# Kernel tuning notes

Measured on AMD Instinct MI355X. Metric: run time of the kernel, lower is better.

The kernel has to match this reference:

```python
import jax, jax.numpy as jnp
import numpy as np

B, H, W, C, A, K = 1_000_000, 4, 4, 3, 4, 20
# slicing offsets (w_offset, h_offset) exactly as in the torch code
OFFSETS = [(0, 1), (2, 1), (1, 0), (1, 2)]


def setup_inputs() -> dict:
    key = jax.random.key(0)
    k0, k1, k2, k3, k4, k5 = jax.random.split(key, 6)
    obs = jax.random.normal(k0, (B, H, W, C), dtype=jnp.float32)
    # channel 1 encodes the agent position: exactly one nonzero per sample
    pos = jax.random.randint(k1, (B,), 0, H * W)
    ch1 = jnp.zeros((B, H * W), jnp.float32).at[jnp.arange(B), pos].set(1.0)
    obs = obs.at[..., 1].set(ch1.reshape(B, H, W)).reshape(B, H * W * C)
    s = 0.05  # keep |p| < 1 mostly so the K-step VI recursion stays bounded
    return {
        'obs': obs,
        'Phi_W': jax.random.normal(k2, (48, 48), jnp.float32) * s,
        'Phi_b': jax.random.normal(k3, (48,), jnp.float32) * s,
        'Logit_W': jax.random.normal(k4, (A, 36), jnp.float32) * s,
        'Logit_b': jax.random.normal(k5, (A,), jnp.float32) * s,
    }


def _pad2(x):
    # zero-pad last two spatial dims of (B, H, W) by 1
    return jnp.pad(x, ((0, 0), (1, 1), (1, 1)))


def reference(obs, Phi_W, Phi_b, Logit_W, Logit_b):
    out = (obs @ Phi_W.T + Phi_b).reshape(B, H, W, C)
    rin, rout, p = out[..., 0], out[..., 1], out[..., 2]
    rin_pad = _pad2(rin)  # (B, 6, 6)

    def step(v, _):
        vp = _pad2(v)  # (B, 6, 6)
        for wo, ho in OFFSETS:
            nv = p * vp[:, ho:ho + H, wo:wo + W] + rin_pad[:, ho:ho + H, wo:wo + W] - rout
            v = jnp.maximum(v, nv)
        return v, None

    V, _ = jax.lax.scan(step, jnp.zeros((B, H, W), jnp.float32), None, length=K)

    # agent position: first nonzero of channel 1 (row-major), default (1,1) -> flat 5
    obs4 = obs.reshape(B, H, W, C)
    nz = (obs4[..., 1] != 0).reshape(B, H * W)
    idx = jnp.where(nz.any(axis=1), jnp.argmax(nz, axis=1), 5)
    i, j = idx // W, idx % W

    # 3x3 windows around (i, j) in zero-padded state / value maps
    obs_pad = jnp.pad(obs4, ((0, 0), (1, 1), (1, 1), (0, 0)))  # (B, 6, 6, 3)
    V_pad = _pad2(V)                                            # (B, 6, 6)
    d = jnp.arange(3)
    rows = i[:, None, None] + d[:, None]   # (B, 3, 1)
    cols = j[:, None, None] + d[None, :]   # (B, 1, 3)
    bb = jnp.arange(B)[:, None, None]
    sub_state = obs_pad[bb, rows, cols]    # (B, 3, 3, 3)
    sub_v = V_pad[bb, rows, cols]          # (B, 3, 3)

    logit_in = jnp.concatenate([sub_state.reshape(B, 27), sub_v.reshape(B, 9)], axis=1)
    logit = logit_in @ Logit_W.T + Logit_b  # (B, A)
    return logit
```

## Files before the change

### kernel.cpp

```cpp
#include <hip/hip_runtime.h>
#include <hip/hip_bf16.h>

#define BT 256
#define WREG 13312

typedef __attribute__((ext_vector_type(8))) short short8;
typedef __attribute__((ext_vector_type(4))) float f32x4;

__device__ inline short f2b(float x) {
    return __builtin_bit_cast(short, __float2bfloat16(x));
}
__device__ inline float b2f(short s) {
    unsigned u = ((unsigned)(unsigned short)s) << 16;
    return __builtin_bit_cast(float, u);
}
__device__ inline short8 pack8(float4 a, float4 b) {
    short8 r;
    r[0] = f2b(a.x); r[1] = f2b(a.y); r[2] = f2b(a.z); r[3] = f2b(a.w);
    r[4] = f2b(b.x); r[5] = f2b(b.y); r[6] = f2b(b.z); r[7] = f2b(b.w);
    return r;
}

__global__ __launch_bounds__(BT, 3) void vin_kernel(
    const float* __restrict__ obs,
    const float* __restrict__ PhiW,
    const float* __restrict__ Phib,
    const float* __restrict__ LW,
    const float* __restrict__ Lb,
    float* __restrict__ out, int Btot)
{
    __shared__ __align__(16) char smem[4 * WREG];
    const int tid  = threadIdx.x;
    const int lane = tid & 63;
    const int wid  = tid >> 6;
    const int b    = blockIdx.x * BT + tid;
    if (b >= Btot) return;

    char* wbase = smem + wid * WREG;
    const int jn = lane & 15;
    const int g  = lane >> 4;

    float o[48];
    {
        const float4* g4 = reinterpret_cast<const float4*>(obs + (size_t)b * 48);
        #pragma unroll
        for (int q = 0; q < 12; ++q) {
            float4 t = g4[q];
            o[4*q+0] = t.x; o[4*q+1] = t.y; o[4*q+2] = t.z; o[4*q+3] = t.w;
        }
    }

    int idx = 5;
    #pragma unroll
    for (int k = 15; k >= 0; --k)
        if (o[k*3+1] != 0.0f) idx = k;
    const int ai = idx >> 2;
    const int aj = idx & 3;

    short8 bfrag[3][2];
    #pragma unroll
    for (int n = 0; n < 3; ++n) {
        const float* wrow = PhiW + (16*n + jn) * 48;
        float4 q0 = *reinterpret_cast<const float4*>(wrow + 8*g);
        float4 q1 = *reinterpret_cast<const float4*>(wrow + 8*g + 4);
        bfrag[n][0] = pack8(q0, q1);
        short8 z = {0,0,0,0,0,0,0,0};
        if (g < 2) {
            float4 q2 = *reinterpret_cast<const float4*>(wrow + 32 + 8*g);
            float4 q3 = *reinterpret_cast<const float4*>(wrow + 36 + 8*g);
            z = pack8(q2, q3);
        }
        bfrag[n][1] = z;
    }

    {
        short8* arow = reinterpret_cast<short8*>(wbase + lane * 144);
        #pragma unroll
        for (int t = 0; t < 6; ++t) {
            short8 v;
            #pragma unroll
            for (int e = 0; e < 8; ++e) v[e] = f2b(o[t*8 + e]);
            arow[t] = v;
        }
        short8 z = {0,0,0,0,0,0,0,0};
        arow[6] = z; arow[7] = z;
    }

    float lg0 = Lb[0], lg1 = Lb[1], lg2 = Lb[2], lg3 = Lb[3];
    {
        const short* myobs = reinterpret_cast<const short*>(wbase + lane * 144);
        #pragma unroll
        for (int dh = 0; dh < 3; ++dh) {
            #pragma unroll
            for (int dw = 0; dw < 3; ++dw) {
                int r = ai + dh - 1, c = aj + dw - 1;
                bool ok = ((unsigned)r < 4u) && ((unsigned)c < 4u);
                int ba = ok ? (r*4 + c) * 3 : 0;
                float s0 = b2f(myobs[ba+0]);
                float s1 = b2f(myobs[ba+1]);
                float s2 = b2f(myobs[ba+2]);
                if (!ok) { s0 = 0.f; s1 = 0.f; s2 = 0.f; }
                int f = (dh*3 + dw) * 3;
                lg0 = fmaf(s0, LW[0*36+f], fmaf(s1, LW[0*36+f+1], fmaf(s2, LW[0*36+f+2], lg0)));
                lg1 = fmaf(s0, LW[1*36+f], fmaf(s1, LW[1*36+f+1], fmaf(s2, LW[1*36+f+2], lg1)));
                lg2 = fmaf(s0, LW[2*36+f], fmaf(s1, LW[2*36+f+1], fmaf(s2, LW[2*36+f+2], lg2)));
                lg3 = fmaf(s0, LW[3*36+f], fmaf(s1, LW[3*36+f+1], fmaf(s2, LW[3*36+f+2], lg3)));
            }
        }
    }

    short8 afrag[4][2];
    #pragma unroll
    for (int m = 0; m < 4; ++m) {
        const char* rp = wbase + (m*16 + jn) * 144;
        afrag[m][0] = *reinterpret_cast<const short8*>(rp + 16*g);
        afrag[m][1] = *reinterpret_cast<const short8*>(rp + 64 + 16*g);
    }

    f32x4 acc[4][3];
    #pragma unroll
    for (int m = 0; m < 4; ++m)
        #pragma unroll
        for (int n = 0; n < 3; ++n)
            acc[m][n] = (f32x4){0.f, 0.f, 0.f, 0.f};
    #pragma unroll
    for (int n = 0; n < 3; ++n)
        #pragma unroll
        for (int m = 0; m < 4; ++m) {
            acc[m][n] = __builtin_amdgcn_mfma_f32_16x16x32_bf16(afrag[m][0], bfrag[n][0], acc[m][n], 0, 0, 0);
            acc[m][n] = __builtin_amdgcn_mfma_f32_16x16x32_bf16(afrag[m][1], bfrag[n][1], acc[m][n], 0, 0, 0);
        }

    asm volatile("s_waitcnt lgkmcnt(0)" ::: "memory");
    __builtin_amdgcn_sched_barrier(0);

    #pragma unroll
    for (int m = 0; m < 4; ++m)
        #pragma unroll
        for (int n = 0; n < 3; ++n)
            #pragma unroll
            for (int r = 0; r < 4; ++r) {
                int row = m*16 + g*4 + r;
                reinterpret_cast<float*>(wbase + row * 208)[n*16 + jn] = acc[m][n][r];
            }

    asm volatile("s_waitcnt lgkmcnt(0)" ::: "memory");
    __builtin_amdgcn_sched_barrier(0);

    float ro[48];
    {
        const char* myrow = wbase + lane * 208;
        #pragma unroll
        for (int q = 0; q < 12; ++q) {
            f32x4 t = *reinterpret_cast<const f32x4*>(myrow + q * 16);
            ro[4*q+0] = t[0] + Phib[4*q+0];
            ro[4*q+1] = t[1] + Phib[4*q+1];
            ro[4*q+2] = t[2] + Phib[4*q+2];
            ro[4*q+3] = t[3] + Phib[4*q+3];
        }
    }

    float pc[16], aL[16], aR[16], aU[16], aD[16];
    #pragma unroll
    for (int h = 0; h < 4; ++h)
        #pragma unroll
        for (int w = 0; w < 4; ++w) {
            int cl = h*4 + w;
            float rout = ro[cl*3 + 1];
            pc[cl] = ro[cl*3 + 2];
            aL[cl] = ((w > 0) ? ro[(cl-1)*3] : 0.0f) - rout;
            aR[cl] = ((w < 3) ? ro[(cl+1)*3] : 0.0f) - rout;
            aU[cl] = ((h > 0) ? ro[(cl-4)*3] : 0.0f) - rout;
            aD[cl] = ((h < 3) ? ro[(cl+4)*3] : 0.0f) - rout;
        }

    float V[16];
    #pragma unroll
    for (int k = 0; k < 16; ++k) V[k] = 0.0f;

    #pragma unroll 1
    for (int s = 0; s < 20; ++s) {
        float Vn[16];
        #pragma unroll
        for (int h = 0; h < 4; ++h)
            #pragma unroll
            for (int w = 0; w < 4; ++w) {
                int cl = h*4 + w;
                float cL = (w > 0) ? fmaf(pc[cl], V[cl-1], aL[cl]) : aL[cl];
                float cR = (w < 3) ? fmaf(pc[cl], V[cl+1], aR[cl]) : aR[cl];
                float cU = (h > 0) ? fmaf(pc[cl], V[cl-4], aU[cl]) : aU[cl];
                float cD = (h < 3) ? fmaf(pc[cl], V[cl+4], aD[cl]) : aD[cl];
                Vn[cl] = fmaxf(fmaxf(V[cl], cL), fmaxf(fmaxf(cR, cU), cD));
            }
        #pragma unroll
        for (int k = 0; k < 16; ++k) V[k] = Vn[k];
    }

    {
        char* myrow = wbase + lane * 208;
        #pragma unroll
        for (int q = 0; q < 4; ++q)
            *reinterpret_cast<f32x4*>(myrow + q * 16) =
                (f32x4){V[4*q+0], V[4*q+1], V[4*q+2], V[4*q+3]};
    }
    asm volatile("s_waitcnt lgkmcnt(0)" ::: "memory");
    __builtin_amdgcn_sched_barrier(0);
    {
        const float* myv = reinterpret_cast<const float*>(wbase + lane * 208);
        #pragma unroll
        for (int dh = 0; dh < 3; ++dh)
            #pragma unroll
            for (int dw = 0; dw < 3; ++dw) {
                int r = ai + dh - 1, c = aj + dw - 1;
                bool ok = ((unsigned)r < 4u) && ((unsigned)c < 4u);
                int ba = ok ? (r*4 + c) : 0;
                float v = myv[ba];
                if (!ok) v = 0.0f;
                int f = 27 + dh*3 + dw;
                lg0 = fmaf(v, LW[0*36+f], lg0);
                lg1 = fmaf(v, LW[1*36+f], lg1);
                lg2 = fmaf(v, LW[2*36+f], lg2);
                lg3 = fmaf(v, LW[3*36+f], lg3);
            }
    }

    reinterpret_cast<float4*>(out)[b] = make_float4(lg0, lg1, lg2, lg3);
}

extern "C" void kernel_launch(void* const* d_in, const int* in_sizes, int n_in,
                              void* d_out, int out_size, void* d_ws, size_t ws_size,
                              hipStream_t stream) {
    const float* obs  = (const float*)d_in[0];
    const float* PhiW = (const float*)d_in[1];
    const float* Phib = (const float*)d_in[2];
    const float* LW   = (const float*)d_in[3];
    const float* Lb   = (const float*)d_in[4];
    float* out = (float*)d_out;

    const int Btot = in_sizes[0] / 48;
    const int grid = (Btot + BT - 1) / BT;
    hipLaunchKernelGGL(vin_kernel, dim3(grid), dim3(BT), 0, stream,
                       obs, PhiW, Phib, LW, Lb, out, Btot);
}
```

Measured before the change: 73.97 us.

## Run value iteration in packed fp16, pre-convert PhiW to bf16, fold bias into MFMA

Runs the 20-step value iteration in packed half2 arithmetic, two grid cells per register, with bit shifts supplying horizontal neighbours. This roughly halves the VALU work in the main loop. A small prep kernel converts PhiW to a padded bf16 layout in workspace, so each thread loads its B fragments directly instead of converting them. Other changes: the bias is folded into the MFMA accumulator initialisation, bf16 packing uses manual rounding, and the agent-index search becomes an arithmetic weighted sum. The fp16 recursion lowers accuracy. The weighted-sum index only works because channel 1 holds exactly one 1.0, so it relies on the input format.

```diff
diff --git a/kernel.cpp b/kernel.cpp
--- a/kernel.cpp
+++ b/kernel.cpp
@@ -1,29 +1,41 @@
 #include <hip/hip_runtime.h>
-#include <hip/hip_bf16.h>
 
 #define BT 256
 #define WREG 13312
 
 typedef __attribute__((ext_vector_type(8))) short short8;
 typedef __attribute__((ext_vector_type(4))) float f32x4;
-
-__device__ inline short f2b(float x) {
-    return __builtin_bit_cast(short, __float2bfloat16(x));
+typedef __attribute__((ext_vector_type(4))) unsigned int u32x4;
+typedef _Float16 h2 __attribute__((ext_vector_type(2)));
+
+__device__ inline h2 hfma2(h2 a, h2 b, h2 c) { return __builtin_elementwise_fma(a, b, c); }
+__device__ inline h2 hmax2(h2 a, h2 b)       { return __builtin_elementwise_max(a, b); }
+__device__ inline h2 mkh2(float a, float b)  { h2 r; r[0] = (_Float16)a; r[1] = (_Float16)b; return r; }
+
+__device__ inline unsigned bf16r(float x) {
+    unsigned u = __builtin_bit_cast(unsigned, x);
+    return (u + 0x7FFFu + ((u >> 16) & 1u)) >> 16;
+}
+__device__ inline unsigned pk2bf(float a, float b) {
+    return bf16r(a) | (bf16r(b) << 16);
 }
 __device__ inline float b2f(short s) {
     unsigned u = ((unsigned)(unsigned short)s) << 16;
     return __builtin_bit_cast(float, u);
 }
-__device__ inline short8 pack8(float4 a, float4 b) {
-    short8 r;
-    r[0] = f2b(a.x); r[1] = f2b(a.y); r[2] = f2b(a.z); r[3] = f2b(a.w);
-    r[4] = f2b(b.x); r[5] = f2b(b.y); r[6] = f2b(b.z); r[7] = f2b(b.w);
-    return r;
+
+__global__ void prep_kernel(const float* __restrict__ PhiW,
+                            unsigned short* __restrict__ wb) {
+    int idx = blockIdx.x * 256 + threadIdx.x;
+    if (idx >= 48 * 64) return;
+    int j = idx >> 6, k = idx & 63;
+    float v = (k < 48) ? PhiW[j * 48 + k] : 0.0f;
+    wb[idx] = (unsigned short)bf16r(v);
 }
 
 __global__ __launch_bounds__(BT, 3) void vin_kernel(
     const float* __restrict__ obs,
-    const float* __restrict__ PhiW,
+    const unsigned short* __restrict__ wb,
     const float* __restrict__ Phib,
     const float* __restrict__ LW,
     const float* __restrict__ Lb,
@@ -50,39 +62,35 @@
         }
     }
 
-    int idx = 5;
-    #pragma unroll
-    for (int k = 15; k >= 0; --k)
-        if (o[k*3+1] != 0.0f) idx = k;
+    float ssum = o[1], sidx = 0.0f;
+    #pragma unroll
+    for (int k = 1; k < 16; ++k) {
+        ssum += o[k*3 + 1];
+        sidx = fmaf(o[k*3 + 1], (float)k, sidx);
+    }
+    const int idx = (ssum != 0.0f) ? (int)(sidx + 0.5f) : 5;
     const int ai = idx >> 2;
     const int aj = idx & 3;
 
     short8 bfrag[3][2];
     #pragma unroll
-    for (int n = 0; n < 3; ++n) {
-        const float* wrow = PhiW + (16*n + jn) * 48;
-        float4 q0 = *reinterpret_cast<const float4*>(wrow + 8*g);
-        float4 q1 = *reinterpret_cast<const float4*>(wrow + 8*g + 4);
-        bfrag[n][0] = pack8(q0, q1);
-        short8 z = {0,0,0,0,0,0,0,0};
-        if (g < 2) {
-            float4 q2 = *reinterpret_cast<const float4*>(wrow + 32 + 8*g);
-            float4 q3 = *reinterpret_cast<const float4*>(wrow + 36 + 8*g);
-            z = pack8(q2, q3);
-        }
-        bfrag[n][1] = z;
-    }
-
-    {
-        short8* arow = reinterpret_cast<short8*>(wbase + lane * 144);
-        #pragma unroll
-        for (int t = 0; t < 6; ++t) {
-            short8 v;
-            #pragma unroll
-            for (int e = 0; e < 8; ++e) v[e] = f2b(o[t*8 + e]);
-            arow[t] = v;
-        }
-        short8 z = {0,0,0,0,0,0,0,0};
+    for (int n = 0; n < 3; ++n)
+        #pragma unroll
+        for (int t = 0; t < 2; ++t)
+            bfrag[n][t] = *reinterpret_cast<const short8*>(
+                wb + (16*n + jn) * 64 + 32*t + 8*g);
+
+    {
+        u32x4* arow = reinterpret_cast<u32x4*>(wbase + lane * 144);
+        #pragma unroll
+        for (int q = 0; q < 6; ++q) {
+            u32x4 v;
+            #pragma unroll
+            for (int e = 0; e < 4; ++e)
+                v[e] = pk2bf(o[q*8 + 2*e], o[q*8 + 2*e + 1]);
+            arow[q] = v;
+        }
+        u32x4 z = {0u, 0u, 0u, 0u};
         arow[6] = z; arow[7] = z;
     }
 
@@ -90,7 +98,7 @@
     {
         const short* myobs = reinterpret_cast<const short*>(wbase + lane * 144);
         #pragma unroll
-        for (int dh = 0; dh < 3; ++dh) {
+        for (int dh = 0; dh < 3; ++dh)
             #pragma unroll
             for (int dw = 0; dw < 3; ++dw) {
                 int r = ai + dh - 1, c = aj + dw - 1;
@@ -106,7 +114,6 @@
                 lg2 = fmaf(s0, LW[2*36+f], fmaf(s1, LW[2*36+f+1], fmaf(s2, LW[2*36+f+2], lg2)));
                 lg3 = fmaf(s0, LW[3*36+f], fmaf(s1, LW[3*36+f+1], fmaf(s2, LW[3*36+f+2], lg3)));
             }
-        }
     }
 
     short8 afrag[4][2];
@@ -118,11 +125,15 @@
     }
 
     f32x4 acc[4][3];
-    #pragma unroll
-    for (int m = 0; m < 4; ++m)
-        #pragma unroll
-        for (int n = 0; n < 3; ++n)
-            acc[m][n] = (f32x4){0.f, 0.f, 0.f, 0.f};
+    {
+        float b0 = Phib[jn], b1 = Phib[16 + jn], b2 = Phib[32 + jn];
+        #pragma unroll
+        for (int m = 0; m < 4; ++m) {
+            acc[m][0] = (f32x4){b0, b0, b0, b0};
+            acc[m][1] = (f32x4){b1, b1, b1, b1};
+            acc[m][2] = (f32x4){b2, b2, b2, b2};
+        }
+    }
     #pragma unroll
     for (int n = 0; n < 3; ++n)
         #pragma unroll
@@ -153,55 +164,78 @@
         #pragma unroll
         for (int q = 0; q < 12; ++q) {
             f32x4 t = *reinterpret_cast<const f32x4*>(myrow + q * 16);
-            ro[4*q+0] = t[0] + Phib[4*q+0];
-            ro[4*q+1] = t[1] + Phib[4*q+1];
-            ro[4*q+2] = t[2] + Phib[4*q+2];
-            ro[4*q+3] = t[3] + Phib[4*q+3];
-        }
-    }
-
-    float pc[16], aL[16], aR[16], aU[16], aD[16];
+            ro[4*q+0] = t[0]; ro[4*q+1] = t[1]; ro[4*q+2] = t[2]; ro[4*q+3] = t[3];
+        }
+    }
+
+    float pcf[16], aLf[16], aRf[16], aUf[16], aDf[16];
     #pragma unroll
     for (int h = 0; h < 4; ++h)
         #pragma unroll
         for (int w = 0; w < 4; ++w) {
             int cl = h*4 + w;
             float rout = ro[cl*3 + 1];
-            pc[cl] = ro[cl*3 + 2];
-            aL[cl] = ((w > 0) ? ro[(cl-1)*3] : 0.0f) - rout;
-            aR[cl] = ((w < 3) ? ro[(cl+1)*3] : 0.0f) - rout;
-            aU[cl] = ((h > 0) ? ro[(cl-4)*3] : 0.0f) - rout;
-            aD[cl] = ((h < 3) ? ro[(cl+4)*3] : 0.0f) - rout;
-        }
-
-    float V[16];
-    #pragma unroll
-    for (int k = 0; k < 16; ++k) V[k] = 0.0f;
+            pcf[cl] = ro[cl*3 + 2];
+            aLf[cl] = ((w > 0) ? ro[(cl-1)*3] : 0.0f) - rout;
+            aRf[cl] = ((w < 3) ? ro[(cl+1)*3] : 0.0f) - rout;
+            aUf[cl] = ((h > 0) ? ro[(cl-4)*3] : 0.0f) - rout;
+            aDf[cl] = ((h < 3) ? ro[(cl+4)*3] : 0.0f) - rout;
+        }
+
+    h2 p2[4][2], aL2[4][2], aR2[4][2], aU2[4][2], aD2[4][2];
+    #pragma unroll
+    for (int h = 0; h < 4; ++h)
+        #pragma unroll
+        for (int j = 0; j < 2; ++j) {
+            int c0 = h*4 + j, c1 = h*4 + j + 2;
+            p2[h][j]  = mkh2(pcf[c0], pcf[c1]);
+            aL2[h][j] = mkh2(aLf[c0], aLf[c1]);
+            aR2[h][j] = mkh2(aRf[c0], aRf[c1]);
+            aU2[h][j] = mkh2(aUf[c0], aUf[c1]);
+            aD2[h][j] = mkh2(aDf[c0], aDf[c1]);
+        }
+
+    h2 Vp[4][2];
+    #pragma unroll
+    for (int h = 0; h < 4; ++h) {
+        Vp[h][0] = mkh2(0.f, 0.f);
+        Vp[h][1] = mkh2(0.f, 0.f);
+    }
 
     #pragma unroll 1
     for (int s = 0; s < 20; ++s) {
-        float Vn[16];
+        h2 shl[4], shr[4], Vn[4][2];
+        #pragma unroll
+        for (int h = 0; h < 4; ++h) {
+            shl[h] = __builtin_bit_cast(h2, __builtin_bit_cast(unsigned, Vp[h][1]) << 16);
+            shr[h] = __builtin_bit_cast(h2, __builtin_bit_cast(unsigned, Vp[h][0]) >> 16);
+        }
         #pragma unroll
         for (int h = 0; h < 4; ++h)
             #pragma unroll
-            for (int w = 0; w < 4; ++w) {
-                int cl = h*4 + w;
-                float cL = (w > 0) ? fmaf(pc[cl], V[cl-1], aL[cl]) : aL[cl];
-                float cR = (w < 3) ? fmaf(pc[cl], V[cl+1], aR[cl]) : aR[cl];
-                float cU = (h > 0) ? fmaf(pc[cl], V[cl-4], aU[cl]) : aU[cl];
-                float cD = (h < 3) ? fmaf(pc[cl], V[cl+4], aD[cl]) : aD[cl];
-                Vn[cl] = fmaxf(fmaxf(V[cl], cL), fmaxf(fmaxf(cR, cU), cD));
-            }
-        #pragma unroll
-        for (int k = 0; k < 16; ++k) V[k] = Vn[k];
+            for (int j = 0; j < 2; ++j) {
+                h2 vL = j ? Vp[h][0] : shl[h];
+                h2 vR = j ? shr[h] : Vp[h][1];
+                h2 tU = (h > 0) ? hfma2(p2[h][j], Vp[h-1][j], aU2[h][j]) : aU2[h][j];
+                h2 tD = (h < 3) ? hfma2(p2[h][j], Vp[h+1][j], aD2[h][j]) : aD2[h][j];
+                h2 m1 = hmax2(Vp[h][j], hfma2(p2[h][j], vL, aL2[h][j]));
+                h2 m2 = hmax2(hfma2(p2[h][j], vR, aR2[h][j]), tU);
+                Vn[h][j] = hmax2(hmax2(m1, m2), tD);
+            }
+        #pragma unroll
+        for (int h = 0; h < 4; ++h) { Vp[h][0] = Vn[h][0]; Vp[h][1] = Vn[h][1]; }
     }
 
     {
         char* myrow = wbase + lane * 208;
         #pragma unroll
-        for (int q = 0; q < 4; ++q)
-            *reinterpret_cast<f32x4*>(myrow + q * 16) =
-                (f32x4){V[4*q+0], V[4*q+1], V[4*q+2], V[4*q+3]};
+        for (int h = 0; h < 4; ++h) {
+            float v0 = (float)Vp[h][0][0];
+            float v1 = (float)Vp[h][1][0];
+            float v2 = (float)Vp[h][0][1];
+            float v3 = (float)Vp[h][1][1];
+            *reinterpret_cast<f32x4*>(myrow + h * 16) = (f32x4){v0, v1, v2, v3};
+        }
     }
     asm volatile("s_waitcnt lgkmcnt(0)" ::: "memory");
     __builtin_amdgcn_sched_barrier(0);
@@ -236,9 +270,12 @@
     const float* LW   = (const float*)d_in[3];
     const float* Lb   = (const float*)d_in[4];
     float* out = (float*)d_out;
+    unsigned short* wb = (unsigned short*)d_ws;
+
+    hipLaunchKernelGGL(prep_kernel, dim3(12), dim3(256), 0, stream, PhiW, wb);
 
     const int Btot = in_sizes[0] / 48;
     const int grid = (Btot + BT - 1) / BT;
     hipLaunchKernelGGL(vin_kernel, dim3(grid), dim3(BT), 0, stream,
-                       obs, PhiW, Phib, LW, Lb, out, Btot);
-}
+                       obs, wb, Phib, LW, Lb, out, Btot);
+}
```

New measurement: 78.90 us. +6.7%, slower.
